# Kernel optimization log

Hardware: AMD Instinct MI355X
Metric: run time of the kernel (lower is better)

## Reference

```python
import jax, jax.numpy as jnp
import numpy as np

N = 50000        # nodes
E = 800000       # edges
F_IN = 128       # num_node_features
H = 128          # hidden_size
C = 128          # num_classes (must be 128 for lin1 to typecheck)
G = 64           # graphs in batch


def setup_inputs() -> dict:
    key = jax.random.key(0)
    ks = jax.random.split(key, 12)
    x = jax.random.normal(ks[0], (N, F_IN), dtype=jnp.float32)
    edge_index = jax.random.randint(ks[1], (2, E), 0, N, dtype=jnp.int64)
    batch = jnp.sort(jax.random.randint(ks[2], (N,), 0, G, dtype=jnp.int64))

    def glorot(k, i, o):
        return jax.random.normal(k, (i, o), dtype=jnp.float32) / np.float32(np.sqrt(i))

    return {
        'x': x, 'edge_index': edge_index, 'batch': batch,
        'W1': glorot(ks[3], F_IN, H), 'b1': jnp.zeros((H,), jnp.float32),
        'W2': glorot(ks[4], H, H),    'b2': jnp.zeros((H,), jnp.float32),
        'W3': glorot(ks[5], H, C),    'b3': jnp.zeros((C,), jnp.float32),
        'Wl': glorot(ks[6], 128, C),  'bl': jnp.zeros((C,), jnp.float32),
    }


def _gcn_conv(x, W, b, src, dst, n):
    # PyG GCNConv: h = x W; out_i = sum_{j->i} d_j^-1/2 d_i^-1/2 h_j + b
    h = x @ W                                                   # [n, out]
    deg = jax.ops.segment_sum(jnp.ones(dst.shape[0], h.dtype), dst, num_segments=n)
    dinv = jnp.where(deg > 0, jax.lax.rsqrt(jnp.maximum(deg, 1.0)), 0.0)
    norm = dinv[src] * dinv[dst]                                # [E+n]
    msg = h[src] * norm[:, None]                                # gather + scale
    return jax.ops.segment_sum(msg, dst, num_segments=n) + b    # scatter-add


def reference(x, edge_index, batch, W1, b1, W2, b2, W3, b3, Wl, bl):
    x = x.astype(jnp.float32)
    loops = jnp.arange(N, dtype=edge_index.dtype)
    src = jnp.concatenate([edge_index[0], loops])  # add self-loops
    dst = jnp.concatenate([edge_index[1], loops])

    h = jax.nn.elu(_gcn_conv(x, W1, b1, src, dst, N))
    h = jax.nn.elu(_gcn_conv(h, W2, b2, src, dst, N))
    h = jax.nn.elu(_gcn_conv(h, W3, b3, src, dst, N))

    # global_mean_pool over batch vector
    cnt = jax.ops.segment_sum(jnp.ones(N, h.dtype), batch, num_segments=G)
    pooled = jax.ops.segment_sum(h, batch, num_segments=G) / jnp.maximum(cnt, 1.0)[:, None]

    # dropout(p=0.2) is identity in eval mode
    return pooled @ Wl + bl
```

## Files before the change

kernel.cpp:

```cpp
#include <hip/hip_runtime.h>
#include <hip/hip_bf16.h>
#include <hip/hip_fp16.h>

#define N_NODES 50000
#define N_GRAPHS 64
#define FILL_CHUNK 4096
#define SLOTS 64
#define SLOT_SHIFT 6
#define PSHIFT 7
#define NPARTS ((N_NODES + 127) >> 7)
#define MM_BLOCKS ((N_NODES + 63) / 64)

typedef _Float16 f16x8 __attribute__((ext_vector_type(8)));
typedef float f32x4 __attribute__((ext_vector_type(4)));


__device__ inline unsigned short f2h_bits(float x) {
    _Float16 h = (_Float16)x;
    return __builtin_bit_cast(unsigned short, h);
}
__device__ inline float h_bits2f(unsigned short b) {
    return (float)__builtin_bit_cast(_Float16, b);
}
__device__ inline unsigned pack_h2(float a, float b) {
    return (unsigned)f2h_bits(a) | ((unsigned)f2h_bits(b) << 16);
}

__device__ inline void fma_h8(float (&acc)[8], uint4 v, float w) {
    acc[0] += w * h_bits2f((unsigned short)(v.x & 0xffffu));
    acc[1] += w * h_bits2f((unsigned short)(v.x >> 16));
    acc[2] += w * h_bits2f((unsigned short)(v.y & 0xffffu));
    acc[3] += w * h_bits2f((unsigned short)(v.y >> 16));
    acc[4] += w * h_bits2f((unsigned short)(v.z & 0xffffu));
    acc[5] += w * h_bits2f((unsigned short)(v.z >> 16));
    acc[6] += w * h_bits2f((unsigned short)(v.w & 0xffffu));
    acc[7] += w * h_bits2f((unsigned short)(v.w >> 16));
}

__device__ inline void aggregate_node(const uint4* __restrict__ hb4,
                                      const int* __restrict__ deg,
                                      const uint4* __restrict__ cvp4,
                                      const float* __restrict__ dinv,
                                      const float* __restrict__ bias,
                                      int node, int li, float (&o)[8]) {
    int dg = min(deg[node], SLOTS);
    int n8 = (dg + 7) >> 3;
    const uint4* bucket = cvp4 + ((size_t)node << (SLOT_SHIFT - 2));
    float di = dinv[node];

    float acc[8];
    #pragma unroll
    for (int i = 0; i < 8; ++i) acc[i] = 0.f;

    uint4 h = hb4[(size_t)node * 16 + li];
    fma_h8(acc, h, di);

    uint4 c0 = make_uint4(0, 0, 0, 0), c1 = c0;
    if (n8 > 0) { c0 = bucket[0]; c1 = bucket[1]; }
    for (int e8 = 0; e8 < n8; ++e8) {
        uint4 nx0 = make_uint4(0, 0, 0, 0), nx1 = nx0;
        if (e8 + 1 < n8) { nx0 = bucket[2 * e8 + 2]; nx1 = bucket[2 * e8 + 3]; }
        uint4 v0 = hb4[(size_t)(c0.x >> 16) * 16 + li];
        uint4 v1 = hb4[(size_t)(c0.y >> 16) * 16 + li];
        uint4 v2 = hb4[(size_t)(c0.z >> 16) * 16 + li];
        uint4 v3 = hb4[(size_t)(c0.w >> 16) * 16 + li];
        uint4 v4 = hb4[(size_t)(c1.x >> 16) * 16 + li];
        uint4 v5 = hb4[(size_t)(c1.y >> 16) * 16 + li];
        uint4 v6 = hb4[(size_t)(c1.z >> 16) * 16 + li];
        uint4 v7 = hb4[(size_t)(c1.w >> 16) * 16 + li];
        fma_h8(acc, v0, h_bits2f((unsigned short)(c0.x & 0xffffu)));
        fma_h8(acc, v1, h_bits2f((unsigned short)(c0.y & 0xffffu)));
        fma_h8(acc, v2, h_bits2f((unsigned short)(c0.z & 0xffffu)));
        fma_h8(acc, v3, h_bits2f((unsigned short)(c0.w & 0xffffu)));
        fma_h8(acc, v4, h_bits2f((unsigned short)(c1.x & 0xffffu)));
        fma_h8(acc, v5, h_bits2f((unsigned short)(c1.y & 0xffffu)));
        fma_h8(acc, v6, h_bits2f((unsigned short)(c1.z & 0xffffu)));
        fma_h8(acc, v7, h_bits2f((unsigned short)(c1.w & 0xffffu)));
        c0 = nx0; c1 = nx1;
    }

    float4 b0 = *(const float4*)&bias[li * 8];
    float4 b1 = *(const float4*)&bias[li * 8 + 4];
    o[0] = di * acc[0] + b0.x; o[1] = di * acc[1] + b0.y;
    o[2] = di * acc[2] + b0.z; o[3] = di * acc[3] + b0.w;
    o[4] = di * acc[4] + b1.x; o[5] = di * acc[5] + b1.y;
    o[6] = di * acc[6] + b1.z; o[7] = di * acc[7] + b1.w;
    #pragma unroll
    for (int i = 0; i < 8; ++i) o[i] = o[i] > 0.f ? o[i] : expm1f(o[i]);
}


__global__ __launch_bounds__(256) void prep_kernel(const int* __restrict__ dst,
                                                   int* __restrict__ cntmat,
                                                   const float* __restrict__ W1,
                                                   const float* __restrict__ W2,
                                                   const float* __restrict__ W3,
                                                   unsigned short* __restrict__ Wt,
                                                   float* __restrict__ pooled,
                                                   int ne, int nch) {
    int blk = blockIdx.x;
    if (blk < nch) {
        __shared__ int h[NPARTS];
        for (int i = threadIdx.x; i < NPARTS; i += 256) h[i] = 0;
        __syncthreads();
        int beg = blk * FILL_CHUNK, end = min(beg + FILL_CHUNK, ne);
        for (int i = beg + threadIdx.x; i < end; i += 256)
            atomicAdd(&h[dst[i] >> PSHIFT], 1);
        __syncthreads();
        for (int i = threadIdx.x; i < NPARTS; i += 256) cntmat[blk * NPARTS + i] = h[i];
    } else if (blk < nch + 192) {
        int i = (blk - nch) * 256 + threadIdx.x;
        int which = i >> 14;
        const float* W = (which == 0) ? W1 : (which == 1) ? W2 : W3;
        int j = i & 16383;
        int nn = j >> 7, k = j & 127;
        Wt[(which << 14) + nn * 128 + k] = f2h_bits(W[k * 128 + nn]);
    } else {
        int i = (blk - nch - 192) * 256 + threadIdx.x;
        if (i < N_GRAPHS * 128) pooled[i] = 0.f;
    }
}


__global__ __launch_bounds__(256) void scanp_mm_kernel(int* __restrict__ cntmat,
                                                       int* __restrict__ ptotal, int nchunks,
                                                       const float* __restrict__ x,
                                                       const unsigned short* __restrict__ Wt,
                                                       unsigned short* __restrict__ Hh, int n) {
    __shared__ unsigned short Wl[128 * 136];
    int blk = blockIdx.x;
    int t = threadIdx.x;

    if (blk < NPARTS) {
        int* s = (int*)Wl;
        int p = blk;
        int v = (t < nchunks) ? cntmat[t * NPARTS + p] : 0;
        s[t] = v;
        __syncthreads();
        #pragma unroll
        for (int d = 1; d < 256; d <<= 1) {
            int y = (t >= d) ? s[t - d] : 0;
            __syncthreads();
            s[t] += y;
            __syncthreads();
        }
        if (t < nchunks) cntmat[t * NPARTS + p] = s[t] - v;
        if (t == 255) ptotal[p] = s[255];
        return;
    }

    {
        int row = t >> 1, seg = t & 1;
        #pragma unroll
        for (int j = 0; j < 8; ++j) {
            int c = seg * 64 + j * 8;
            *(uint4*)&Wl[row * 136 + c] = *(const uint4*)&Wt[row * 128 + c];
        }
    }
    __syncthreads();

    int w = t >> 6, lane = t & 63;
    int lm = lane & 15, lg = lane >> 4;
    int r0 = (blk - NPARTS) * 64 + w * 16;

    f32x4 acc[8];
    #pragma unroll
    for (int ct = 0; ct < 8; ++ct) acc[ct] = (f32x4){0.f, 0.f, 0.f, 0.f};

    int ar = min(r0 + lm, n - 1);

    #pragma unroll
    for (int kk = 0; kk < 4; ++kk) {
        const float* arow = x + (size_t)ar * 128;
        float4 lo = *(const float4*)&arow[kk * 32 + lg * 8];
        float4 hi = *(const float4*)&arow[kk * 32 + lg * 8 + 4];
        f16x8 a;
        a[0] = (_Float16)lo.x; a[1] = (_Float16)lo.y;
        a[2] = (_Float16)lo.z; a[3] = (_Float16)lo.w;
        a[4] = (_Float16)hi.x; a[5] = (_Float16)hi.y;
        a[6] = (_Float16)hi.z; a[7] = (_Float16)hi.w;
        #pragma unroll
        for (int ct = 0; ct < 8; ++ct) {
            f16x8 b = *(const f16x8*)&Wl[(ct * 16 + lm) * 136 + kk * 32 + lg * 8];
            acc[ct] = __builtin_amdgcn_mfma_f32_16x16x32_f16(a, b, acc[ct], 0, 0, 0);
        }
    }

    #pragma unroll
    for (int ct = 0; ct < 8; ++ct) {
        #pragma unroll
        for (int i = 0; i < 4; ++i) {
            int rr = r0 + lg * 4 + i;
            if (rr < n) Hh[(size_t)rr * 128 + ct * 16 + lm] = f2h_bits(acc[ct][i]);
        }
    }
}

__global__ __launch_bounds__(512) void scant_kernel(const int* __restrict__ ptotal,
                                                    int* __restrict__ pbase) {
    __shared__ int s[512];
    int t = threadIdx.x;
    int v = (t < NPARTS) ? ptotal[t] : 0;
    s[t] = v;
    __syncthreads();
    #pragma unroll
    for (int d = 1; d < 512; d <<= 1) {
        int y = (t >= d) ? s[t - d] : 0;
        __syncthreads();
        s[t] += y;
        __syncthreads();
    }
    if (t < NPARTS) pbase[t] = s[t] - v;
    if (t == NPARTS - 1) pbase[NPARTS] = s[t];
}

__global__ __launch_bounds__(256) void bin_scatter_kernel(const int* __restrict__ src,
                                                          const int* __restrict__ dst,
                                                          const int* __restrict__ cntmat,
                                                          const int* __restrict__ pbase,
                                                          unsigned* __restrict__ binned, int ne) {
    __shared__ int pos[NPARTS];
    int c = blockIdx.x, t = threadIdx.x;
    for (int i = t; i < NPARTS; i += 256) pos[i] = pbase[i] + cntmat[c * NPARTS + i];
    __syncthreads();
    int beg = c * FILL_CHUNK, end = min(beg + FILL_CHUNK, ne);
    for (int i = beg + t; i < end; i += 256) {
        int d = dst[i];
        int p = d >> PSHIFT;
        int idx = atomicAdd(&pos[p], 1);
        binned[idx] = ((unsigned)(d & 127) << 16) | (unsigned)src[i];
    }
}

__global__ __launch_bounds__(256) void bucket_fill_kernel(const unsigned* __restrict__ binned,
                                                          const int* __restrict__ pbase,
                                                          int* __restrict__ deg,
                                                          float* __restrict__ dinv,
                                                          unsigned* __restrict__ tag,
                                                          uint4* __restrict__ cvp4, int n) {
    __shared__ unsigned bkt[128 * SLOTS];
    __shared__ int curls[128];
    int p = blockIdx.x, t = threadIdx.x;
    if (t < 128) curls[t] = 0;
    __syncthreads();
    int beg = pbase[p], end = pbase[p + 1];
    for (int i = beg + t; i < end; i += 256) {
        unsigned e = binned[i];
        int dl = (int)(e >> 16);
        int ps = atomicAdd(&curls[dl], 1);
        if (ps < SLOTS) bkt[(dl << SLOT_SHIFT) + ps] = e & 0xFFFFu;
    }
    __syncthreads();
    int node0 = p << PSHIFT;
    if (t < 128 && node0 + t < n) {
        int c = curls[t];
        deg[node0 + t] = c;
        float dv = rsqrtf((float)c + 1.0f);
        dinv[node0 + t] = dv;
        tag[node0 + t] = ((unsigned)(node0 + t) << 16) | (unsigned)f2h_bits(dv);
    }
    const uint4* b4 = (const uint4*)bkt;
    uint4* outp = cvp4 + (size_t)p * (128 * SLOTS / 4);
    for (int i = t; i < 128 * SLOTS / 4; i += 256) outp[i] = b4[i];
}

__global__ __launch_bounds__(256) void tagify_kernel(const int* __restrict__ deg,
                                                     const unsigned* __restrict__ tag,
                                                     uint4* __restrict__ cvp4, int n) {
    int t = blockIdx.x * 256 + threadIdx.x;
    int node = t >> 4;
    if (node >= n) return;
    int slot0 = (t & 15) << 2;
    int dg = min(deg[node], SLOTS);
    int lim = (dg + 7) & ~7;
    if (slot0 >= lim) return;
    uint4 v = cvp4[t];
    uint4 r;
    r.x = (slot0     < dg) ? tag[v.x & 0xFFFFu] : 0u;
    r.y = (slot0 + 1 < dg) ? tag[v.y & 0xFFFFu] : 0u;
    r.z = (slot0 + 2 < dg) ? tag[v.z & 0xFFFFu] : 0u;
    r.w = (slot0 + 3 < dg) ? tag[v.w & 0xFFFFu] : 0u;
    cvp4[t] = r;
}


__global__ __launch_bounds__(256) void fused_agg_mm_kernel(const uint4* __restrict__ hb4,
                                                           const int* __restrict__ deg,
                                                           const uint4* __restrict__ cvp4,
                                                           const float* __restrict__ dinv,
                                                           const float* __restrict__ bias,
                                                           const unsigned short* __restrict__ Wt,
                                                           unsigned short* __restrict__ Hh,
                                                           int n) {
    __shared__ unsigned short Wl[128 * 136];
    __shared__ unsigned short actl[16 * 136];
    int t = threadIdx.x;

    {
        int row = t >> 1, seg = t & 1;
        #pragma unroll
        for (int j = 0; j < 8; ++j) {
            int c = seg * 64 + j * 8;
            *(uint4*)&Wl[row * 136 + c] = *(const uint4*)&Wt[row * 128 + c];
        }
    }

    int nl = t >> 4;
    int li = t & 15;
    int node = blockIdx.x * 16 + nl;

    float o[8];
    aggregate_node(hb4, deg, cvp4, dinv, bias, node, li, o);

    uint4 pk;
    pk.x = pack_h2(o[0], o[1]);
    pk.y = pack_h2(o[2], o[3]);
    pk.z = pack_h2(o[4], o[5]);
    pk.w = pack_h2(o[6], o[7]);
    *(uint4*)&actl[nl * 136 + li * 8] = pk;

    __syncthreads();

    int w = t >> 6, lane = t & 63;
    int lm = lane & 15, lg = lane >> 4;

    f32x4 macc[2];
    macc[0] = (f32x4){0.f, 0.f, 0.f, 0.f};
    macc[1] = (f32x4){0.f, 0.f, 0.f, 0.f};

    #pragma unroll
    for (int kk = 0; kk < 4; ++kk) {
        f16x8 a = *(const f16x8*)&actl[lm * 136 + kk * 32 + lg * 8];
        #pragma unroll
        for (int j = 0; j < 2; ++j) {
            int ct = w * 2 + j;
            f16x8 b = *(const f16x8*)&Wl[(ct * 16 + lm) * 136 + kk * 32 + lg * 8];
            macc[j] = __builtin_amdgcn_mfma_f32_16x16x32_f16(a, b, macc[j], 0, 0, 0);
        }
    }

    #pragma unroll
    for (int j = 0; j < 2; ++j) {
        int ct = w * 2 + j;
        #pragma unroll
        for (int i = 0; i < 4; ++i) {
            int rr = blockIdx.x * 16 + lg * 4 + i;
            Hh[(size_t)rr * 128 + ct * 16 + lm] = f2h_bits(macc[j][i]);
        }
    }
}


__global__ __launch_bounds__(256) void fused_agg_pool_kernel(const uint4* __restrict__ hb4,
                                                             const int* __restrict__ deg,
                                                             const uint4* __restrict__ cvp4,
                                                             const float* __restrict__ dinv,
                                                             const float* __restrict__ bias,
                                                             const int* __restrict__ batch,
                                                             float* __restrict__ pooled,
                                                             int n) {
    __shared__ float plds[16][132];
    __shared__ int gid[16];
    int t = threadIdx.x;
    int nl = t >> 4;
    int li = t & 15;
    int node = blockIdx.x * 16 + nl;

    if (t < 16) gid[t] = batch[blockIdx.x * 16 + t];

    float o[8];
    aggregate_node(hb4, deg, cvp4, dinv, bias, node, li, o);

    #pragma unroll
    for (int i = 0; i < 8; ++i) plds[nl][li * 8 + i] = o[i];

    __syncthreads();

    int f = t & 127, rg = t >> 7;
    int r0 = rg * 8;
    float local = 0.f;
    int gprev = gid[r0];
    #pragma unroll
    for (int r = r0; r < r0 + 8; ++r) {
        int g = gid[r];
        if (g != gprev) {
            atomicAdd(&pooled[gprev * 128 + f], local);
            local = 0.f;
            gprev = g;
        }
        local += plds[r][f];
    }
    atomicAdd(&pooled[gprev * 128 + f], local);
}


__global__ __launch_bounds__(128) void linear_kernel(const float* __restrict__ pooled,
                                                     const int* __restrict__ batch,
                                                     const float* __restrict__ Wl,
                                                     const float* __restrict__ bl,
                                                     float* __restrict__ out, int n) {
    __shared__ float p[128];
    int g = blockIdx.x, t = threadIdx.x;

    int lo = 0, hi = n;
    while (lo < hi) { int m = (lo + hi) >> 1; if (batch[m] < g) lo = m + 1; else hi = m; }
    int s0 = lo;
    hi = n;
    while (lo < hi) { int m = (lo + hi) >> 1; if (batch[m] < g + 1) lo = m + 1; else hi = m; }
    int e0 = lo;
    float cntf = (float)max(e0 - s0, 1);

    p[t] = pooled[g * 128 + t] / cntf;
    __syncthreads();
    float acc = bl[t];
    for (int k = 0; k < 128; ++k) acc += p[k] * Wl[k * 128 + t];
    out[g * 128 + t] = acc;
}


extern "C" void kernel_launch(void* const* d_in, const int* in_sizes, int n_in,
                              void* d_out, int out_size, void* d_ws, size_t ws_size,
                              hipStream_t stream) {
    const float* x     = (const float*)d_in[0];
    const int*   ei    = (const int*)d_in[1];
    const int*   batch = (const int*)d_in[2];
    const float* W1 = (const float*)d_in[3];
    const float* b1 = (const float*)d_in[4];
    const float* W2 = (const float*)d_in[5];
    const float* b2 = (const float*)d_in[6];
    const float* W3 = (const float*)d_in[7];
    const float* b3 = (const float*)d_in[8];
    const float* Wl = (const float*)d_in[9];
    const float* bl = (const float*)d_in[10];
    float* out = (float*)d_out;

    const int N_ = N_NODES;
    const int E_ = in_sizes[1] / 2;
    const int G_ = N_GRAPHS;
    const int* src = ei;
    const int* dst = ei + E_;
    const int NCH = (E_ + FILL_CHUNK - 1) / FILL_CHUNK;

    char* ws = (char*)d_ws;
    size_t off = 0;
    auto alloc = [&](size_t bytes) -> char* {
        char* p = ws + off;
        off += (bytes + 255) & ~(size_t)255;
        return p;
    };

    float*          dinv   = (float*)          alloc((size_t)N_ * 4);
    unsigned*       tag    = (unsigned*)       alloc((size_t)N_ * 4);
    int*            deg    = (int*)            alloc((size_t)N_ * 4);
    int*            cntmat = (int*)            alloc((size_t)NCH * NPARTS * 4);
    int*            ptotal = (int*)            alloc((size_t)NPARTS * 4);
    int*            pbase  = (int*)            alloc((size_t)(NPARTS + 1) * 4);
    unsigned*       binned = (unsigned*)       alloc((size_t)E_ * 4);
    unsigned*       cvp    = (unsigned*)       alloc((size_t)NPARTS * 128 * SLOTS * 4);
    unsigned short* hbuf   = (unsigned short*) alloc((size_t)N_ * 128 * 2);
    unsigned short* hbuf2  = (unsigned short*) alloc((size_t)N_ * 128 * 2);
    unsigned short* wt     = (unsigned short*) alloc(3 * 128 * 128 * 2);
    float*          pooled = (float*)          alloc((size_t)G_ * 128 * 4);
    (void)ws_size;

    int agblocks = (N_ + 15) / 16;

    prep_kernel<<<NCH + 192 + 32, 256, 0, stream>>>(dst, cntmat, W1, W2, W3, wt, pooled, E_, NCH);
    scanp_mm_kernel<<<NPARTS + MM_BLOCKS, 256, 0, stream>>>(cntmat, ptotal, NCH, x, wt, hbuf, N_);
    scant_kernel<<<1, 512, 0, stream>>>(ptotal, pbase);
    bin_scatter_kernel<<<NCH, 256, 0, stream>>>(src, dst, cntmat, pbase, binned, E_);
    bucket_fill_kernel<<<NPARTS, 256, 0, stream>>>(binned, pbase, deg, dinv, tag, (uint4*)cvp, N_);
    tagify_kernel<<<(N_ * 16 + 255) / 256, 256, 0, stream>>>(deg, tag, (uint4*)cvp, N_);

    fused_agg_mm_kernel<<<agblocks, 256, 0, stream>>>((const uint4*)hbuf, deg, (const uint4*)cvp,
                                                      dinv, b1, wt + 16384, hbuf2, N_);
    fused_agg_mm_kernel<<<agblocks, 256, 0, stream>>>((const uint4*)hbuf2, deg, (const uint4*)cvp,
                                                      dinv, b2, wt + 32768, hbuf, N_);
    fused_agg_pool_kernel<<<agblocks, 256, 0, stream>>>((const uint4*)hbuf, deg, (const uint4*)cvp,
                                                        dinv, b3, batch, pooled, N_);

    linear_kernel<<<G_, 128, 0, stream>>>(pooled, batch, Wl, bl, out, N_);
}
```

Before: 168.2 us.

## Fuse neighbor tagging into first aggregation+matmul kernel, trim bucket copy-out

Removes the separate tagify kernel and does the tag lookup inside the first layer's aggregation kernel. Each block tags its 16 nodes' buckets, writes them back for later layers, and stages them in shared memory for the gather loop. The bucket fill kernel now copies only the occupied slots of each node's bucket instead of the whole fixed-size bucket. This saves one launch and a full read/write pass over the bucket array. In exchange the first aggregation kernel takes an extra dependent tag gather and a block barrier before its gathers. The new kernel reads Wt straight from global memory rather than through shared memory.

```diff
diff --git a/kernel.cpp b/kernel.cpp
--- a/kernel.cpp
+++ b/kernel.cpp
@@ -37,24 +37,9 @@
     acc[7] += w * h_bits2f((unsigned short)(v.w >> 16));
 }
 
-__device__ inline void aggregate_node(const uint4* __restrict__ hb4,
-                                      const int* __restrict__ deg,
-                                      const uint4* __restrict__ cvp4,
-                                      const float* __restrict__ dinv,
-                                      const float* __restrict__ bias,
-                                      int node, int li, float (&o)[8]) {
-    int dg = min(deg[node], SLOTS);
-    int n8 = (dg + 7) >> 3;
-    const uint4* bucket = cvp4 + ((size_t)node << (SLOT_SHIFT - 2));
-    float di = dinv[node];
-
-    float acc[8];
-    #pragma unroll
-    for (int i = 0; i < 8; ++i) acc[i] = 0.f;
-
-    uint4 h = hb4[(size_t)node * 16 + li];
-    fma_h8(acc, h, di);
-
+template<typename BUCKET>
+__device__ inline void agg_loop(const uint4* __restrict__ hb4, BUCKET bucket, int n8,
+                                int li, float (&acc)[8]) {
     uint4 c0 = make_uint4(0, 0, 0, 0), c1 = c0;
     if (n8 > 0) { c0 = bucket[0]; c1 = bucket[1]; }
     for (int e8 = 0; e8 < n8; ++e8) {
@@ -78,7 +63,10 @@
         fma_h8(acc, v7, h_bits2f((unsigned short)(c1.w & 0xffffu)));
         c0 = nx0; c1 = nx1;
     }
-
+}
+
+__device__ inline void bias_elu(const float* __restrict__ bias, float di, int li,
+                                float (&acc)[8], float (&o)[8]) {
     float4 b0 = *(const float4*)&bias[li * 8];
     float4 b1 = *(const float4*)&bias[li * 8 + 4];
     o[0] = di * acc[0] + b0.x; o[1] = di * acc[1] + b0.y;
@@ -87,6 +75,26 @@
     o[6] = di * acc[6] + b1.z; o[7] = di * acc[7] + b1.w;
     #pragma unroll
     for (int i = 0; i < 8; ++i) o[i] = o[i] > 0.f ? o[i] : expm1f(o[i]);
+}
+
+__device__ inline void aggregate_node(const uint4* __restrict__ hb4,
+                                      const int* __restrict__ deg,
+                                      const uint4* __restrict__ cvp4,
+                                      const float* __restrict__ dinv,
+                                      const float* __restrict__ bias,
+                                      int node, int li, float (&o)[8]) {
+    int dg = min(deg[node], SLOTS);
+    int n8 = (dg + 7) >> 3;
+    const uint4* bucket = cvp4 + ((size_t)node << (SLOT_SHIFT - 2));
+    float di = dinv[node];
+
+    float acc[8];
+    #pragma unroll
+    for (int i = 0; i < 8; ++i) acc[i] = 0.f;
+    uint4 h = hb4[(size_t)node * 16 + li];
+    fma_h8(acc, h, di);
+    agg_loop(hb4, bucket, n8, li, acc);
+    bias_elu(bias, di, li, acc, o);
 }
 
 
@@ -259,28 +267,100 @@
         dinv[node0 + t] = dv;
         tag[node0 + t] = ((unsigned)(node0 + t) << 16) | (unsigned)f2h_bits(dv);
     }
+    __syncthreads();
     const uint4* b4 = (const uint4*)bkt;
     uint4* outp = cvp4 + (size_t)p * (128 * SLOTS / 4);
-    for (int i = t; i < 128 * SLOTS / 4; i += 256) outp[i] = b4[i];
-}
-
-__global__ __launch_bounds__(256) void tagify_kernel(const int* __restrict__ deg,
-                                                     const unsigned* __restrict__ tag,
-                                                     uint4* __restrict__ cvp4, int n) {
-    int t = blockIdx.x * 256 + threadIdx.x;
-    int node = t >> 4;
-    if (node >= n) return;
-    int slot0 = (t & 15) << 2;
+    for (int i = t; i < 128 * (SLOTS / 4); i += 256) {
+        int r = i >> 4, s4 = i & 15;
+        int lim4 = ((min(curls[r], SLOTS) + 7) & ~7) >> 2;
+        if (s4 < lim4) outp[i] = b4[i];
+    }
+}
+
+
+__global__ __launch_bounds__(256) void fused_tag_agg_mm_kernel(const uint4* __restrict__ hb4,
+                                                               const int* __restrict__ deg,
+                                                               const unsigned* __restrict__ tag,
+                                                               uint4* __restrict__ cvp4,
+                                                               const float* __restrict__ dinv,
+                                                               const float* __restrict__ bias,
+                                                               const unsigned short* __restrict__ Wt,
+                                                               unsigned short* __restrict__ Hh,
+                                                               int n) {
+    __shared__ uint4 bkt4[16 * 16];
+    __shared__ unsigned short actl[16 * 136];
+    int t = threadIdx.x;
+    int nl = t >> 4;
+    int li = t & 15;
+    int node = blockIdx.x * 16 + nl;
+
+    {
+        int slot0 = li << 2;
+        int dgn = min(deg[node], SLOTS);
+        int lim = (dgn + 7) & ~7;
+        uint4 r = make_uint4(0, 0, 0, 0);
+        if (slot0 < lim) {
+            uint4 v = cvp4[(size_t)node * 16 + li];
+            r.x = (slot0     < dgn) ? tag[v.x & 0xFFFFu] : 0u;
+            r.y = (slot0 + 1 < dgn) ? tag[v.y & 0xFFFFu] : 0u;
+            r.z = (slot0 + 2 < dgn) ? tag[v.z & 0xFFFFu] : 0u;
+            r.w = (slot0 + 3 < dgn) ? tag[v.w & 0xFFFFu] : 0u;
+            cvp4[(size_t)node * 16 + li] = r;
+        }
+        bkt4[nl * 16 + li] = r;
+    }
+    __syncthreads();
+
     int dg = min(deg[node], SLOTS);
-    int lim = (dg + 7) & ~7;
-    if (slot0 >= lim) return;
-    uint4 v = cvp4[t];
-    uint4 r;
-    r.x = (slot0     < dg) ? tag[v.x & 0xFFFFu] : 0u;
-    r.y = (slot0 + 1 < dg) ? tag[v.y & 0xFFFFu] : 0u;
-    r.z = (slot0 + 2 < dg) ? tag[v.z & 0xFFFFu] : 0u;
-    r.w = (slot0 + 3 < dg) ? tag[v.w & 0xFFFFu] : 0u;
-    cvp4[t] = r;
+    int n8 = (dg + 7) >> 3;
+    float di = dinv[node];
+
+    float acc[8];
+    #pragma unroll
+    for (int i = 0; i < 8; ++i) acc[i] = 0.f;
+    uint4 h = hb4[(size_t)node * 16 + li];
+    fma_h8(acc, h, di);
+    agg_loop(hb4, (const uint4*)&bkt4[nl * 16], n8, li, acc);
+
+    float o[8];
+    bias_elu(bias, di, li, acc, o);
+
+    uint4 pk;
+    pk.x = pack_h2(o[0], o[1]);
+    pk.y = pack_h2(o[2], o[3]);
+    pk.z = pack_h2(o[4], o[5]);
+    pk.w = pack_h2(o[6], o[7]);
+    *(uint4*)&actl[nl * 136 + li * 8] = pk;
+
+    __syncthreads();
+
+    int w = t >> 6, lane = t & 63;
+    int lm = lane & 15, lg = lane >> 4;
+
+    f32x4 macc[2];
+    macc[0] = (f32x4){0.f, 0.f, 0.f, 0.f};
+    macc[1] = (f32x4){0.f, 0.f, 0.f, 0.f};
+
+    #pragma unroll
+    for (int kk = 0; kk < 4; ++kk) {
+        f16x8 a = *(const f16x8*)&actl[lm * 136 + kk * 32 + lg * 8];
+        #pragma unroll
+        for (int j = 0; j < 2; ++j) {
+            int ct = w * 2 + j;
+            f16x8 b = *(const f16x8*)&Wt[(size_t)(ct * 16 + lm) * 128 + kk * 32 + lg * 8];
+            macc[j] = __builtin_amdgcn_mfma_f32_16x16x32_f16(a, b, macc[j], 0, 0, 0);
+        }
+    }
+
+    #pragma unroll
+    for (int j = 0; j < 2; ++j) {
+        int ct = w * 2 + j;
+        #pragma unroll
+        for (int i = 0; i < 4; ++i) {
+            int rr = blockIdx.x * 16 + lg * 4 + i;
+            Hh[(size_t)rr * 128 + ct * 16 + lm] = f2h_bits(macc[j][i]);
+        }
+    }
 }
 
 
@@ -470,10 +550,9 @@
     scant_kernel<<<1, 512, 0, stream>>>(ptotal, pbase);
     bin_scatter_kernel<<<NCH, 256, 0, stream>>>(src, dst, cntmat, pbase, binned, E_);
     bucket_fill_kernel<<<NPARTS, 256, 0, stream>>>(binned, pbase, deg, dinv, tag, (uint4*)cvp, N_);
-    tagify_kernel<<<(N_ * 16 + 255) / 256, 256, 0, stream>>>(deg, tag, (uint4*)cvp, N_);
-
-    fused_agg_mm_kernel<<<agblocks, 256, 0, stream>>>((const uint4*)hbuf, deg, (const uint4*)cvp,
-                                                      dinv, b1, wt + 16384, hbuf2, N_);
+
+    fused_tag_agg_mm_kernel<<<agblocks, 256, 0, stream>>>((const uint4*)hbuf, deg, tag, (uint4*)cvp,
+                                                          dinv, b1, wt + 16384, hbuf2, N_);
     fused_agg_mm_kernel<<<agblocks, 256, 0, stream>>>((const uint4*)hbuf2, deg, (const uint4*)cvp,
                                                       dinv, b2, wt + 32768, hbuf, N_);
     fused_agg_pool_kernel<<<agblocks, 256, 0, stream>>>((const uint4*)hbuf, deg, (const uint4*)cvp,
```

Result: faster. 164.2 us (-2.4%).
